# Kernel optimization log

Hardware: AMD Instinct MI355X
Metric: run time of the kernel (lower is better)

Reference implementation:

```python
import jax, jax.numpy as jnp
import numpy as np

B, N, DIM = 8, 512, 768
H, DH = 12, 64
INNER = H * DH
MLP = 3072
DEPTH = 4
EPS = 1e-5
LS = 0.1  # LayerScale init_eps for depth <= 18


def _ln(x, scale):
    # flax LayerNorm(use_bias=False): (x-mean)/sqrt(var+eps) * scale
    mu = jnp.mean(x, axis=-1, keepdims=True)
    var = jnp.mean(jnp.square(x - mu), axis=-1, keepdims=True)
    return (x - mu) * jax.lax.rsqrt(var + EPS) * scale


def setup_inputs() -> dict:
    key = jax.random.key(0)
    ks = jax.random.split(key, 13)
    s = 0.02
    inp = {
        "x": jax.random.normal(ks[0], (B, N, DIM), jnp.float32),
        "ln1": jnp.ones((DEPTH, DIM), jnp.float32),
        "Wq": jax.random.normal(ks[1], (DEPTH, DIM, INNER), jnp.float32) * s,
        "Wkv": jax.random.normal(ks[2], (DEPTH, DIM, 2 * INNER), jnp.float32) * s,
        "mix_pre": jax.random.normal(ks[3], (DEPTH, H, H), jnp.float32) * 0.1,
        "mix_post": jax.random.normal(ks[4], (DEPTH, H, H), jnp.float32) * 0.1,
        "Wo": jax.random.normal(ks[5], (DEPTH, INNER, DIM), jnp.float32) * s,
        "bo": jnp.zeros((DEPTH, DIM), jnp.float32),
        "ln2": jnp.ones((DEPTH, DIM), jnp.float32),
        "W1": jax.random.normal(ks[6], (DEPTH, DIM, MLP), jnp.float32) * s,
        "b1": jnp.zeros((DEPTH, MLP), jnp.float32),
        "W2": jax.random.normal(ks[7], (DEPTH, MLP, DIM), jnp.float32) * s,
        "b2": jnp.zeros((DEPTH, DIM), jnp.float32),
    }
    return inp


def _block(x, p):
    ln1, Wq, Wkv, mp, mq, Wo, bo, ln2, W1, b1, W2, b2 = p
    scale = DH ** -0.5
    h = _ln(x, ln1)
    q = h @ Wq                                  # [b,n,inner]
    kv = h @ Wkv
    k, v = jnp.split(kv, 2, axis=-1)
    def to_heads(t):
        return t.reshape(B, N, H, DH).transpose(0, 2, 1, 3)  # b h n d
    q, k, v = to_heads(q), to_heads(k), to_heads(v)
    dots = jnp.einsum('bhid,bhjd->bhij', q, k) * scale
    dots = jnp.einsum('bhij,hg->bgij', dots, mp)   # talking-heads pre-softmax
    attn = jax.nn.softmax(dots, axis=-1)
    attn = jnp.einsum('bhij,hg->bgij', attn, mq)   # talking-heads post-softmax
    o = jnp.einsum('bhij,bhjd->bhid', attn, v)
    o = o.transpose(0, 2, 1, 3).reshape(B, N, INNER)
    x = (o @ Wo + bo) * LS + x
    h2 = _ln(x, ln2)
    x = ((jax.nn.gelu(h2 @ W1 + b1) @ W2) + b2) * LS + x
    return x, None


def reference(x, ln1, Wq, Wkv, mix_pre, mix_post, Wo, bo, ln2, W1, b1, W2, b2):
    params = (ln1, Wq, Wkv, mix_pre, mix_post, Wo, bo, ln2, W1, b1, W2, b2)
    out, _ = jax.lax.scan(_block, x, params)
    return out
```

## Files before the change

kernel.cpp:

```cpp
#include <hip/hip_runtime.h>


#define LSCALE 0.1f

typedef __bf16 bf16;
typedef __bf16 bf16x8 __attribute__((ext_vector_type(8)));
typedef unsigned short ushort4v __attribute__((ext_vector_type(4)));
typedef float  f32x4  __attribute__((ext_vector_type(4)));

__device__ __forceinline__ void g2l16(const void* g, void* l) {
    __builtin_amdgcn_global_load_lds(
        (const __attribute__((address_space(1))) void*)g,
        (__attribute__((address_space(3))) void*)l, 16, 0, 0);
}

template<int EPI>
__global__ __launch_bounds__(256, 2)
void gemm_bt(const bf16* __restrict__ A, int lda, long saz1, long saz2,
             const bf16* __restrict__ Bt, int ldb, long sbz1, long sbz2,
             void* __restrict__ Cv, int ldc, long scz1, long scz2,
             int M, int N, int K, int zmod,
             const float* __restrict__ bias, float scale)
{
    __shared__ __align__(16) char smem[35840];
    bf16* As = (bf16*)smem;
    bf16* Bs = (bf16*)(smem + 16384);
    bf16* Cs = (bf16*)smem;

    const int z  = blockIdx.z;
    const int z1 = z / zmod, z2 = z - z1 * zmod;
    const bf16* Ab = A  + saz1 * (long)z1 + saz2 * (long)z2;
    const bf16* Bb = Bt + sbz1 * (long)z1 + sbz2 * (long)z2;

    const int m0 = blockIdx.x * 128, n0 = blockIdx.y * 128;
    const int tid = threadIdx.x, w = tid >> 6, l = tid & 63;
    const int wr = (w >> 1) * 64, wc = (w & 1) * 64;
    const int lr = l & 15, lq = l >> 4;
    const int srow = l >> 2, scol8 = (l & 3) * 8;

    f32x4 acc[4][4];
#pragma unroll
    for (int i = 0; i < 4; i++)
#pragma unroll
        for (int j = 0; j < 4; j++)
#pragma unroll
            for (int r = 0; r < 4; r++) acc[i][j][r] = 0.f;

    for (int k0 = 0; k0 < K; k0 += 64) {
        const bf16* Ag = Ab + (long)(m0 + w * 32) * lda + k0;
        const bf16* Bg = Bb + (long)(n0 + w * 32) * ldb + k0;
        g2l16(Ag + (long)srow * lda + scol8,             As + w * 1024);
        g2l16(Ag + (long)(srow + 16) * lda + scol8,      As + w * 1024 + 512);
        g2l16(Ag + (long)srow * lda + 32 + scol8,        As + 4096 + w * 1024);
        g2l16(Ag + (long)(srow + 16) * lda + 32 + scol8, As + 4096 + w * 1024 + 512);
        g2l16(Bg + (long)srow * ldb + scol8,             Bs + w * 1024);
        g2l16(Bg + (long)(srow + 16) * ldb + scol8,      Bs + w * 1024 + 512);
        g2l16(Bg + (long)srow * ldb + 32 + scol8,        Bs + 4096 + w * 1024);
        g2l16(Bg + (long)(srow + 16) * ldb + 32 + scol8, Bs + 4096 + w * 1024 + 512);
        __syncthreads();

#pragma unroll
        for (int hh = 0; hh < 2; hh++) {
            bf16x8 fa[4], fb[4];
#pragma unroll
            for (int i = 0; i < 4; i++)
                fa[i] = *(const bf16x8*)(As + hh * 4096 + (wr + i * 16 + lr) * 32 + lq * 8);
#pragma unroll
            for (int i = 0; i < 4; i++)
                fb[i] = *(const bf16x8*)(Bs + hh * 4096 + (wc + i * 16 + lr) * 32 + lq * 8);
#pragma unroll
            for (int mi = 0; mi < 4; mi++)
#pragma unroll
                for (int ni = 0; ni < 4; ni++)
                    acc[mi][ni] = __builtin_amdgcn_mfma_f32_16x16x32_bf16(
                        fa[mi], fb[ni], acc[mi][ni], 0, 0, 0);
        }
        __syncthreads();
    }

#pragma unroll
    for (int ni = 0; ni < 4; ni++) {
        const int col = wc + ni * 16 + lr;
        float bv = 0.f;
        if (EPI == 1) bv = bias[n0 + col];
#pragma unroll
        for (int mi = 0; mi < 4; mi++) {
#pragma unroll
            for (int r = 0; r < 4; r++) {
                const int row = wr + mi * 16 + lq * 4 + r;
                float v = acc[mi][ni][r];
                if (EPI == 0) {
                    v *= scale;
                } else if (EPI == 1) {
                    const float xx = v + bv;
                    const float u  = 0.7978845608f * (xx + 0.044715f * xx * xx * xx);
                    const float th = 1.f - 2.f / (__expf(2.f * u) + 1.f);
                    v = 0.5f * xx * (1.f + th);
                }
                Cs[row * 136 + col] = (bf16)v;
            }
        }
    }
    __syncthreads();

    const long cb = scz1 * (long)z1 + scz2 * (long)z2;
    const int rrow = tid >> 4, cg = tid & 15;
#pragma unroll
    for (int p = 0; p < 8; p++) {
        const int row = p * 16 + rrow;
        const bf16x8 v = *(const bf16x8*)(Cs + row * 136 + cg * 8);
        *(bf16x8*)((bf16*)Cv + cb + (long)(m0 + row) * ldc + n0 + cg * 8) = v;
    }
}

__global__ __launch_bounds__(256, 2)
void gemm_av(const bf16* __restrict__ S, const bf16* __restrict__ qkvc,
             bf16* __restrict__ oc)
{
    __shared__ __align__(16) bf16 As[128 * 32];
    __shared__ __align__(16) bf16 Bst[64 * 40];

    const int z = blockIdx.y, b = z / 12, g = z - b * 12;
    const bf16* Ab = S + (long)z * 262144;
    const bf16* Bb = qkvc + (long)b * 1179648 + 1536 + g * 64;
    bf16* Cb = oc + (long)b * 1179648 + g * 64;

    const int i0 = blockIdx.x * 128;
    const int tid = threadIdx.x, w = tid >> 6, l = tid & 63;
    const int lr = l & 15, lq = l >> 4;
    const int srow = l >> 2, scol8 = (l & 3) * 8;
    const int kp = tid >> 4, dq = tid & 15;
    const int kcol = ((((kp >> 2) ^ ((dq >> 1) & 3)) << 3) | ((kp & 3) << 1));

    f32x4 acc[2][4];
#pragma unroll
    for (int i = 0; i < 2; i++)
#pragma unroll
        for (int j = 0; j < 4; j++)
#pragma unroll
            for (int r = 0; r < 4; r++) acc[i][j][r] = 0.f;

    bf16* Al = As + w * 1024;
    unsigned short* Bw = (unsigned short*)Bst;

    for (int k0 = 0; k0 < 512; k0 += 32) {
        const bf16* Ag = Ab + (long)(i0 + w * 32) * 512 + k0;
        g2l16(Ag + (long)srow * 512 + scol8,        Al);
        g2l16(Ag + (long)(srow + 16) * 512 + scol8, Al + 512);

        const bf16* Bg = Bb + (long)(k0 + 2 * kp) * 2304 + dq * 4;
        ushort4v u0 = *(const ushort4v*)(Bg);
        ushort4v u1 = *(const ushort4v*)(Bg + 2304);
#pragma unroll
        for (int r = 0; r < 4; r++) {
            unsigned p = (unsigned)u0[r] | ((unsigned)u1[r] << 16);
            *(unsigned*)(Bw + (dq * 4 + r) * 40 + kcol) = p;
        }
        __syncthreads();

        bf16x8 fa[2], fb[4];
#pragma unroll
        for (int i = 0; i < 2; i++)
            fa[i] = *(const bf16x8*)(As + (w * 32 + i * 16 + lr) * 32 + lq * 8);
#pragma unroll
        for (int i = 0; i < 4; i++) {
            const int d = i * 16 + lr;
            fb[i] = *(const bf16x8*)(Bst + d * 40 + ((lq ^ ((d >> 3) & 3)) << 3));
        }
#pragma unroll
        for (int mi = 0; mi < 2; mi++)
#pragma unroll
            for (int ni = 0; ni < 4; ni++)
                acc[mi][ni] = __builtin_amdgcn_mfma_f32_16x16x32_bf16(
                    fa[mi], fb[ni], acc[mi][ni], 0, 0, 0);
        __syncthreads();
    }

#pragma unroll
    for (int ni = 0; ni < 4; ni++) {
        const int gc = ni * 16 + lr;
#pragma unroll
        for (int mi = 0; mi < 2; mi++)
#pragma unroll
            for (int r = 0; r < 4; r++) {
                const int gr = i0 + w * 32 + mi * 16 + lq * 4 + r;
                Cb[(long)gr * 2304 + gc] = (bf16)acc[mi][ni][r];
            }
    }
}

__global__ __launch_bounds__(256)
void tconv_k(const float* __restrict__ in, bf16* __restrict__ out,
             int K, int N)
{
    __shared__ float t[32][33];
    const int n0 = blockIdx.x * 32, k0 = blockIdx.y * 32;
    const int x = threadIdx.x, y = threadIdx.y;
#pragma unroll
    for (int yy = 0; yy < 4; yy++)
        t[y + yy * 8][x] = in[(long)(k0 + y + yy * 8) * N + n0 + x];
    __syncthreads();
#pragma unroll
    for (int yy = 0; yy < 4; yy++)
        out[(long)(n0 + y + yy * 8) * K + k0 + x] = (bf16)t[x][y + yy * 8];
}

__global__ __launch_bounds__(256)
void lnres_k(float* __restrict__ xf, const bf16* __restrict__ P0,
             const bf16* __restrict__ P1, const float* __restrict__ bias,
             const float* __restrict__ gam, bf16* __restrict__ out)
{
    const int row = blockIdx.x, t = threadIdx.x;
    float* xr = xf + (long)row * 768;
    float v[3];
#pragma unroll
    for (int i = 0; i < 3; i++) {
        const int c = t + i * 256;
        float xv = xr[c];
        if (P0) {
            xv += LSCALE * ((float)P0[(long)row * 768 + c] +
                            (float)P1[(long)row * 768 + c] + bias[c]);
            xr[c] = xv;
        }
        v[i] = xv;
    }
    float s  = v[0] + v[1] + v[2];
    float ss = v[0] * v[0] + v[1] * v[1] + v[2] * v[2];
#pragma unroll
    for (int off = 32; off; off >>= 1) {
        s  += __shfl_xor(s, off);
        ss += __shfl_xor(ss, off);
    }
    __shared__ float ps[4], pss[4];
    const int wv = t >> 6, l = t & 63;
    if (l == 0) { ps[wv] = s; pss[wv] = ss; }
    __syncthreads();
    s  = ps[0] + ps[1] + ps[2] + ps[3];
    ss = pss[0] + pss[1] + pss[2] + pss[3];
    const float mu = s * (1.f / 768.f);
    const float rs = rsqrtf(ss * (1.f / 768.f) - mu * mu + 1e-5f);
    bf16* orow = out + (long)row * 768;
#pragma unroll
    for (int i = 0; i < 3; i++) {
        const int c = t + i * 256;
        orow[c] = (bf16)((v[i] - mu) * rs * gam[c]);
    }
}

__global__ __launch_bounds__(256)
void outres_k(const float* __restrict__ xf, const bf16* __restrict__ P0,
              const bf16* __restrict__ P1, const float* __restrict__ bias,
              float* __restrict__ out)
{
    const long i = (long)blockIdx.x * 256 + threadIdx.x;
    const int c = (int)(i % 768);
    out[i] = xf[i] + LSCALE * ((float)P0[i] + (float)P1[i] + bias[c]);
}

__global__ __launch_bounds__(256)
void mixsm_k(bf16* __restrict__ S, const float* __restrict__ mp,
             const float* __restrict__ mq)
{
    __shared__ float buf[12][512];
    __shared__ float rds[12];
    const int b = blockIdx.y, i = blockIdx.x, t = threadIdx.x;
    bf16* Sb = S + ((long)b * 12 * 512 + i) * 512;

    float s0[12], s1[12];
#pragma unroll
    for (int h = 0; h < 12; h++) {
        union { unsigned u; bf16 v[2]; } p;
        p.u = *(const unsigned*)(Sb + (long)h * 262144 + 2 * t);
        s0[h] = (float)p.v[0];
        s1[h] = (float)p.v[1];
    }
#pragma unroll
    for (int g = 0; g < 12; g++) {
        float a0 = 0.f, a1 = 0.f;
#pragma unroll
        for (int h = 0; h < 12; h++) {
            const float m = mp[h * 12 + g];
            a0 += s0[h] * m;
            a1 += s1[h] * m;
        }
        *(float2*)(&buf[g][2 * t]) = make_float2(a0, a1);
    }
    __syncthreads();

    const int wv = t >> 6, l = t & 63;
    for (int g = wv; g < 12; g += 4) {
        float mx = -3.0e38f;
#pragma unroll
        for (int k = 0; k < 8; k++) mx = fmaxf(mx, buf[g][l + 64 * k]);
#pragma unroll
        for (int off = 32; off; off >>= 1) mx = fmaxf(mx, __shfl_xor(mx, off));
        float sm = 0.f;
#pragma unroll
        for (int k = 0; k < 8; k++) {
            const float e = __expf(buf[g][l + 64 * k] - mx);
            buf[g][l + 64 * k] = e;
            sm += e;
        }
#pragma unroll
        for (int off = 32; off; off >>= 1) sm += __shfl_xor(sm, off);
        if (l == 0) rds[g] = 1.f / sm;
    }
    __syncthreads();

    float e0[12], e1[12];
#pragma unroll
    for (int h = 0; h < 12; h++) {
        const float2 ee = *(const float2*)(&buf[h][2 * t]);
        const float rd = rds[h];
        e0[h] = ee.x * rd;
        e1[h] = ee.y * rd;
    }
#pragma unroll
    for (int g = 0; g < 12; g++) {
        float a0 = 0.f, a1 = 0.f;
#pragma unroll
        for (int h = 0; h < 12; h++) {
            const float m = mq[h * 12 + g];
            a0 += e0[h] * m;
            a1 += e1[h] * m;
        }
        union { unsigned u; bf16 v[2]; } p;
        p.v[0] = (bf16)a0;
        p.v[1] = (bf16)a1;
        *(unsigned*)(Sb + (long)g * 262144 + 2 * t) = p.u;
    }
}

extern "C" void kernel_launch(void* const* d_in, const int* in_sizes, int n_in,
                              void* d_out, int out_size, void* d_ws, size_t ws_size,
                              hipStream_t stream)
{
    (void)in_sizes; (void)n_in; (void)out_size; (void)ws_size;
    const float* x   = (const float*)d_in[0];
    const float* ln1 = (const float*)d_in[1];
    const float* Wq  = (const float*)d_in[2];
    const float* Wkv = (const float*)d_in[3];
    const float* mp  = (const float*)d_in[4];
    const float* mq  = (const float*)d_in[5];
    const float* Wo  = (const float*)d_in[6];
    const float* bo  = (const float*)d_in[7];
    const float* ln2 = (const float*)d_in[8];
    const float* W1  = (const float*)d_in[9];
    const float* b1  = (const float*)d_in[10];
    const float* W2  = (const float*)d_in[11];
    const float* b2  = (const float*)d_in[12];

    char* ws = (char*)d_ws;
    float* xf  = (float*)(ws);
    bf16* h    = (bf16*)(ws + 12582912);
    bf16* qkv  = (bf16*)(ws + 18874368);
    bf16* S    = (bf16*)(ws + 37748736);
    bf16* Wt   = (bf16*)(ws + 62914560);
    bf16* mid  = S;
    bf16* P0   = h;
    bf16* P1w2 = qkv;
    bf16* P1wo = S;
    const long P1W2_OFF = 3145728;
    const long P1WO_OFF = 12582912;

    const dim3 tb(32, 8);

    hipMemcpyAsync(xf, x, 4096 * 768 * sizeof(float),
                   hipMemcpyDeviceToDevice, stream);

    for (int L = 0; L < 4; L++) {
        tconv_k<<<dim3(24, 24), tb, 0, stream>>>(Wq + (long)L * 589824, Wt, 768, 768);
        tconv_k<<<dim3(48, 24), tb, 0, stream>>>(Wkv + (long)L * 1179648, Wt + 589824, 768, 1536);

        if (L == 0)
            lnres_k<<<4096, 256, 0, stream>>>(xf, nullptr, nullptr, nullptr,
                                              ln1 + L * 768, h);
        else
            lnres_k<<<4096, 256, 0, stream>>>(xf, P0, P1w2, b2 + (L - 1) * 768,
                                              ln1 + L * 768, h);

        gemm_bt<0><<<dim3(32, 18, 1), 256, 0, stream>>>(
            h, 768, 0, 0, Wt, 768, 0, 0,
            qkv, 2304, 0, 0, 4096, 2304, 768, 1, nullptr, 1.f);

        for (int c = 0; c < 2; c++) {
            const long qb = (long)c * 4718592;
            gemm_bt<0><<<dim3(4, 4, 48), 256, 0, stream>>>(
                qkv + qb,       2304, 1179648, 64,
                qkv + 768 + qb, 2304, 1179648, 64,
                S,               512, 3145728, 262144,
                512, 512, 64, 12, nullptr, 0.125f);

            mixsm_k<<<dim3(512, 4), 256, 0, stream>>>(S, mp + L * 144, mq + L * 144);

            gemm_av<<<dim3(4, 48), 256, 0, stream>>>(S, qkv + qb, qkv + qb);
        }

        tconv_k<<<dim3(24, 24), tb, 0, stream>>>(Wo + (long)L * 589824, Wt, 768, 768);
        gemm_bt<4><<<dim3(32, 6, 2), 256, 0, stream>>>(
            qkv, 2304, 0, 384, Wt, 768, 0, 384,
            P0, 768, 0, P1WO_OFF, 4096, 768, 384, 2, nullptr, 1.f);

        lnres_k<<<4096, 256, 0, stream>>>(xf, P0, P1wo, bo + L * 768,
                                          ln2 + L * 768, h);

        tconv_k<<<dim3(96, 24), tb, 0, stream>>>(W1 + (long)L * 2359296, Wt, 768, 3072);
        gemm_bt<1><<<dim3(32, 24, 1), 256, 0, stream>>>(
            h, 768, 0, 0, Wt, 768, 0, 0,
            mid, 3072, 0, 0, 4096, 3072, 768, 1, b1 + L * 3072, 1.f);

        tconv_k<<<dim3(24, 96), tb, 0, stream>>>(W2 + (long)L * 2359296, Wt, 3072, 768);
        gemm_bt<4><<<dim3(32, 6, 2), 256, 0, stream>>>(
            mid, 3072, 0, 1536, Wt, 3072, 0, 1536,
            P0, 768, 0, P1W2_OFF, 4096, 768, 1536, 2, nullptr, 1.f);
    }

    outres_k<<<12288, 256, 0, stream>>>(xf, P0, P1w2, b2 + 3 * 768, (float*)d_out);
}
```

Measured before the change: 1.022 ms.

## Batch all weight transposes into one launch and process attention for all batches at once

```diff
diff --git a/kernel.cpp b/kernel.cpp
--- a/kernel.cpp
+++ b/kernel.cpp
@@ -113,11 +113,11 @@
     }
 }
 
-__global__ __launch_bounds__(256, 2)
+__global__ __launch_bounds__(256, 4)
 void gemm_av(const bf16* __restrict__ S, const bf16* __restrict__ qkvc,
              bf16* __restrict__ oc)
 {
-    __shared__ __align__(16) bf16 As[128 * 32];
+    __shared__ __align__(16) bf16 As[64 * 32];
     __shared__ __align__(16) bf16 Bst[64 * 40];
 
     const int z = blockIdx.y, b = z / 12, g = z - b * 12;
@@ -125,28 +125,24 @@
     const bf16* Bb = qkvc + (long)b * 1179648 + 1536 + g * 64;
     bf16* Cb = oc + (long)b * 1179648 + g * 64;
 
-    const int i0 = blockIdx.x * 128;
+    const int i0 = blockIdx.x * 64;
     const int tid = threadIdx.x, w = tid >> 6, l = tid & 63;
     const int lr = l & 15, lq = l >> 4;
     const int srow = l >> 2, scol8 = (l & 3) * 8;
     const int kp = tid >> 4, dq = tid & 15;
     const int kcol = ((((kp >> 2) ^ ((dq >> 1) & 3)) << 3) | ((kp & 3) << 1));
 
-    f32x4 acc[2][4];
-#pragma unroll
-    for (int i = 0; i < 2; i++)
-#pragma unroll
-        for (int j = 0; j < 4; j++)
-#pragma unroll
-            for (int r = 0; r < 4; r++) acc[i][j][r] = 0.f;
-
-    bf16* Al = As + w * 1024;
+    f32x4 acc[4];
+#pragma unroll
+    for (int j = 0; j < 4; j++)
+#pragma unroll
+        for (int r = 0; r < 4; r++) acc[j][r] = 0.f;
+
     unsigned short* Bw = (unsigned short*)Bst;
 
     for (int k0 = 0; k0 < 512; k0 += 32) {
-        const bf16* Ag = Ab + (long)(i0 + w * 32) * 512 + k0;
-        g2l16(Ag + (long)srow * 512 + scol8,        Al);
-        g2l16(Ag + (long)(srow + 16) * 512 + scol8, Al + 512);
+        const bf16* Ag = Ab + (long)(i0 + w * 16) * 512 + k0;
+        g2l16(Ag + (long)srow * 512 + scol8, As + w * 512);
 
         const bf16* Bg = Bb + (long)(k0 + 2 * kp) * 2304 + dq * 4;
         ushort4v u0 = *(const ushort4v*)(Bg);
@@ -158,21 +154,17 @@
         }
         __syncthreads();
 
-        bf16x8 fa[2], fb[4];
-#pragma unroll
-        for (int i = 0; i < 2; i++)
-            fa[i] = *(const bf16x8*)(As + (w * 32 + i * 16 + lr) * 32 + lq * 8);
+        bf16x8 fa = *(const bf16x8*)(As + (w * 16 + lr) * 32 + lq * 8);
+        bf16x8 fb[4];
 #pragma unroll
         for (int i = 0; i < 4; i++) {
             const int d = i * 16 + lr;
             fb[i] = *(const bf16x8*)(Bst + d * 40 + ((lq ^ ((d >> 3) & 3)) << 3));
         }
 #pragma unroll
-        for (int mi = 0; mi < 2; mi++)
-#pragma unroll
-            for (int ni = 0; ni < 4; ni++)
-                acc[mi][ni] = __builtin_amdgcn_mfma_f32_16x16x32_bf16(
-                    fa[mi], fb[ni], acc[mi][ni], 0, 0, 0);
+        for (int ni = 0; ni < 4; ni++)
+            acc[ni] = __builtin_amdgcn_mfma_f32_16x16x32_bf16(
+                fa, fb[ni], acc[ni], 0, 0, 0);
         __syncthreads();
     }
 
@@ -180,12 +172,10 @@
     for (int ni = 0; ni < 4; ni++) {
         const int gc = ni * 16 + lr;
 #pragma unroll
-        for (int mi = 0; mi < 2; mi++)
-#pragma unroll
-            for (int r = 0; r < 4; r++) {
-                const int gr = i0 + w * 32 + mi * 16 + lq * 4 + r;
-                Cb[(long)gr * 2304 + gc] = (bf16)acc[mi][ni][r];
-            }
+        for (int r = 0; r < 4; r++) {
+            const int gr = i0 + w * 16 + lq * 4 + r;
+            Cb[(long)gr * 2304 + gc] = (bf16)acc[ni][r];
+        }
     }
 }
 
@@ -203,6 +193,42 @@
 #pragma unroll
     for (int yy = 0; yy < 4; yy++)
         out[(long)(n0 + y + yy * 8) * K + k0 + x] = (bf16)t[x][y + yy * 8];
+}
+
+__global__ __launch_bounds__(256)
+void tconv_all(const float* __restrict__ Wq, const float* __restrict__ Wkv,
+               const float* __restrict__ Wo, const float* __restrict__ W1,
+               const float* __restrict__ W2, bf16* __restrict__ WtAll)
+{
+    __shared__ float t[32][33];
+    const int L = blockIdx.y;
+    bf16* WtL = WtAll + (long)L * 7077888;
+    int bx = blockIdx.x;
+    const float* src; bf16* dst; int K, N, ntx;
+    if (bx < 576) {
+        src = Wq + (long)L * 589824;   dst = WtL;            K = 768;  N = 768;  ntx = 24;
+    } else if (bx < 1728) {
+        bx -= 576;
+        src = Wkv + (long)L * 1179648; dst = WtL + 589824;   K = 768;  N = 1536; ntx = 48;
+    } else if (bx < 2304) {
+        bx -= 1728;
+        src = Wo + (long)L * 589824;   dst = WtL + 1769472;  K = 768;  N = 768;  ntx = 24;
+    } else if (bx < 4608) {
+        bx -= 2304;
+        src = W1 + (long)L * 2359296;  dst = WtL + 2359296;  K = 768;  N = 3072; ntx = 96;
+    } else {
+        bx -= 4608;
+        src = W2 + (long)L * 2359296;  dst = WtL + 4718592;  K = 3072; N = 768;  ntx = 24;
+    }
+    const int n0 = (bx % ntx) * 32, k0 = (bx / ntx) * 32;
+    const int x = threadIdx.x, y = threadIdx.y;
+#pragma unroll
+    for (int yy = 0; yy < 4; yy++)
+        t[y + yy * 8][x] = src[(long)(k0 + y + yy * 8) * N + n0 + x];
+    __syncthreads();
+#pragma unroll
+    for (int yy = 0; yy < 4; yy++)
+        dst[(long)(n0 + y + yy * 8) * K + k0 + x] = (bf16)t[x][y + yy * 8];
 }
 
 __global__ __launch_bounds__(256)
@@ -335,7 +361,7 @@
                               void* d_out, int out_size, void* d_ws, size_t ws_size,
                               hipStream_t stream)
 {
-    (void)in_sizes; (void)n_in; (void)out_size; (void)ws_size;
+    (void)in_sizes; (void)n_in; (void)out_size;
     const float* x   = (const float*)d_in[0];
     const float* ln1 = (const float*)d_in[1];
     const float* Wq  = (const float*)d_in[2];
@@ -355,7 +381,6 @@
     bf16* h    = (bf16*)(ws + 12582912);
     bf16* qkv  = (bf16*)(ws + 18874368);
     bf16* S    = (bf16*)(ws + 37748736);
-    bf16* Wt   = (bf16*)(ws + 62914560);
     bf16* mid  = S;
     bf16* P0   = h;
     bf16* P1w2 = qkv;
@@ -368,51 +393,99 @@
     hipMemcpyAsync(xf, x, 4096 * 768 * sizeof(float),
                    hipMemcpyDeviceToDevice, stream);
 
-    for (int L = 0; L < 4; L++) {
-        tconv_k<<<dim3(24, 24), tb, 0, stream>>>(Wq + (long)L * 589824, Wt, 768, 768);
-        tconv_k<<<dim3(48, 24), tb, 0, stream>>>(Wkv + (long)L * 1179648, Wt + 589824, 768, 1536);
-
-        if (L == 0)
-            lnres_k<<<4096, 256, 0, stream>>>(xf, nullptr, nullptr, nullptr,
-                                              ln1 + L * 768, h);
-        else
-            lnres_k<<<4096, 256, 0, stream>>>(xf, P0, P1w2, b2 + (L - 1) * 768,
-                                              ln1 + L * 768, h);
-
-        gemm_bt<0><<<dim3(32, 18, 1), 256, 0, stream>>>(
-            h, 768, 0, 0, Wt, 768, 0, 0,
-            qkv, 2304, 0, 0, 4096, 2304, 768, 1, nullptr, 1.f);
-
-        for (int c = 0; c < 2; c++) {
-            const long qb = (long)c * 4718592;
-            gemm_bt<0><<<dim3(4, 4, 48), 256, 0, stream>>>(
-                qkv + qb,       2304, 1179648, 64,
-                qkv + 768 + qb, 2304, 1179648, 64,
-                S,               512, 3145728, 262144,
+    if (ws_size >= 144703488ull) {
+        bf16* WtAll = (bf16*)(ws + 88080384);
+
+        tconv_all<<<dim3(6912, 4), tb, 0, stream>>>(Wq, Wkv, Wo, W1, W2, WtAll);
+
+        for (int L = 0; L < 4; L++) {
+            bf16* WtL = WtAll + (long)L * 7077888;
+
+            if (L == 0)
+                lnres_k<<<4096, 256, 0, stream>>>(xf, nullptr, nullptr, nullptr,
+                                                  ln1 + L * 768, h);
+            else
+                lnres_k<<<4096, 256, 0, stream>>>(xf, P0, P1w2, b2 + (L - 1) * 768,
+                                                  ln1 + L * 768, h);
+
+            gemm_bt<0><<<dim3(32, 18, 1), 256, 0, stream>>>(
+                h, 768, 0, 0, WtL, 768, 0, 0,
+                qkv, 2304, 0, 0, 4096, 2304, 768, 1, nullptr, 1.f);
+
+            gemm_bt<0><<<dim3(4, 4, 96), 256, 0, stream>>>(
+                qkv,       2304, 1179648, 64,
+                qkv + 768, 2304, 1179648, 64,
+                S,          512, 3145728, 262144,
                 512, 512, 64, 12, nullptr, 0.125f);
 
-            mixsm_k<<<dim3(512, 4), 256, 0, stream>>>(S, mp + L * 144, mq + L * 144);
-
-            gemm_av<<<dim3(4, 48), 256, 0, stream>>>(S, qkv + qb, qkv + qb);
-        }
-
-        tconv_k<<<dim3(24, 24), tb, 0, stream>>>(Wo + (long)L * 589824, Wt, 768, 768);
-        gemm_bt<4><<<dim3(32, 6, 2), 256, 0, stream>>>(
-            qkv, 2304, 0, 384, Wt, 768, 0, 384,
-            P0, 768, 0, P1WO_OFF, 4096, 768, 384, 2, nullptr, 1.f);
-
-        lnres_k<<<4096, 256, 0, stream>>>(xf, P0, P1wo, bo + L * 768,
-                                          ln2 + L * 768, h);
-
-        tconv_k<<<dim3(96, 24), tb, 0, stream>>>(W1 + (long)L * 2359296, Wt, 768, 3072);
-        gemm_bt<1><<<dim3(32, 24, 1), 256, 0, stream>>>(
-            h, 768, 0, 0, Wt, 768, 0, 0,
-            mid, 3072, 0, 0, 4096, 3072, 768, 1, b1 + L * 3072, 1.f);
-
-        tconv_k<<<dim3(24, 96), tb, 0, stream>>>(W2 + (long)L * 2359296, Wt, 3072, 768);
-        gemm_bt<4><<<dim3(32, 6, 2), 256, 0, stream>>>(
-            mid, 3072, 0, 1536, Wt, 3072, 0, 1536,
-            P0, 768, 0, P1W2_OFF, 4096, 768, 1536, 2, nullptr, 1.f);
+            mixsm_k<<<dim3(512, 8), 256, 0, stream>>>(S, mp + L * 144, mq + L * 144);
+
+            gemm_av<<<dim3(8, 96), 256, 0, stream>>>(S, qkv, qkv);
+
+            gemm_bt<4><<<dim3(32, 6, 2), 256, 0, stream>>>(
+                qkv, 2304, 0, 384, WtL + 1769472, 768, 0, 384,
+                P0, 768, 0, P1WO_OFF, 4096, 768, 384, 2, nullptr, 1.f);
+
+            lnres_k<<<4096, 256, 0, stream>>>(xf, P0, P1wo, bo + L * 768,
+                                              ln2 + L * 768, h);
+
+            gemm_bt<1><<<dim3(32, 24, 1), 256, 0, stream>>>(
+                h, 768, 0, 0, WtL + 2359296, 768, 0, 0,
+                mid, 3072, 0, 0, 4096, 3072, 768, 1, b1 + L * 3072, 1.f);
+
+            gemm_bt<4><<<dim3(32, 6, 2), 256, 0, stream>>>(
+                mid, 3072, 0, 1536, WtL + 4718592, 3072, 0, 1536,
+                P0, 768, 0, P1W2_OFF, 4096, 768, 1536, 2, nullptr, 1.f);
+        }
+    } else {
+        bf16* Wt = (bf16*)(ws + 62914560);
+
+        for (int L = 0; L < 4; L++) {
+            tconv_k<<<dim3(24, 24), tb, 0, stream>>>(Wq + (long)L * 589824, Wt, 768, 768);
+            tconv_k<<<dim3(48, 24), tb, 0, stream>>>(Wkv + (long)L * 1179648, Wt + 589824, 768, 1536);
+
+            if (L == 0)
+                lnres_k<<<4096, 256, 0, stream>>>(xf, nullptr, nullptr, nullptr,
+                                                  ln1 + L * 768, h);
+            else
+                lnres_k<<<4096, 256, 0, stream>>>(xf, P0, P1w2, b2 + (L - 1) * 768,
+                                                  ln1 + L * 768, h);
+
+            gemm_bt<0><<<dim3(32, 18, 1), 256, 0, stream>>>(
+                h, 768, 0, 0, Wt, 768, 0, 0,
+                qkv, 2304, 0, 0, 4096, 2304, 768, 1, nullptr, 1.f);
+
+            for (int c = 0; c < 2; c++) {
+                const long qb = (long)c * 4718592;
+                gemm_bt<0><<<dim3(4, 4, 48), 256, 0, stream>>>(
+                    qkv + qb,       2304, 1179648, 64,
+                    qkv + 768 + qb, 2304, 1179648, 64,
+                    S,               512, 3145728, 262144,
+                    512, 512, 64, 12, nullptr, 0.125f);
+
+                mixsm_k<<<dim3(512, 4), 256, 0, stream>>>(S, mp + L * 144, mq + L * 144);
+
+                gemm_av<<<dim3(8, 48), 256, 0, stream>>>(S, qkv + qb, qkv + qb);
+            }
+
+            tconv_k<<<dim3(24, 24), tb, 0, stream>>>(Wo + (long)L * 589824, Wt, 768, 768);
+            gemm_bt<4><<<dim3(32, 6, 2), 256, 0, stream>>>(
+                qkv, 2304, 0, 384, Wt, 768, 0, 384,
+                P0, 768, 0, P1WO_OFF, 4096, 768, 384, 2, nullptr, 1.f);
+
+            lnres_k<<<4096, 256, 0, stream>>>(xf, P0, P1wo, bo + L * 768,
+                                              ln2 + L * 768, h);
+
+            tconv_k<<<dim3(96, 24), tb, 0, stream>>>(W1 + (long)L * 2359296, Wt, 768, 3072);
+            gemm_bt<1><<<dim3(32, 24, 1), 256, 0, stream>>>(
+                h, 768, 0, 0, Wt, 768, 0, 0,
+                mid, 3072, 0, 0, 4096, 3072, 768, 1, b1 + L * 3072, 1.f);
+
+            tconv_k<<<dim3(24, 96), tb, 0, stream>>>(W2 + (long)L * 2359296, Wt, 3072, 768);
+            gemm_bt<4><<<dim3(32, 6, 2), 256, 0, stream>>>(
+                mid, 3072, 0, 1536, Wt, 3072, 0, 1536,
+                P0, 768, 0, P1W2_OFF, 4096, 768, 1536, 2, nullptr, 1.f);
+        }
     }
 
     outres_k<<<12288, 256, 0, stream>>>(xf, P0, P1w2, b2 + 3 * 768, (float*)d_out);
```

Result: faster. 889.6 us (-12.9%).
